# Kernel optimization log

Measured on AMD Instinct MI355X. Metric: run time of the kernel, lower is better.

## Reference

```python
import jax, jax.numpy as jnp
import numpy as np

B, D, OUT = 16384, 128, 32

def setup_inputs() -> dict:
    key = jax.random.key(0)
    kx, kw, kb = jax.random.split(key, 3)
    x = jax.random.normal(kx, (B, D), dtype=jnp.float32)
    # nn.Linear(in=D*(D+1), out=OUT): weight [OUT, D*(D+1)], bias [OUT]
    fan_in = D * (D + 1)
    bound = 1.0 / np.sqrt(fan_in)
    W = jax.random.uniform(kw, (OUT, fan_in), dtype=jnp.float32, minval=-bound, maxval=bound)
    b = jax.random.uniform(kb, (OUT,), dtype=jnp.float32, minval=-bound, maxval=bound)
    return {"x": x, "W": W, "b": b}

def reference(x, W, b):
    Bn, d = x.shape
    ones = jnp.ones((Bn, 1), dtype=x.dtype)
    xe = jnp.concatenate([x, ones], axis=-1)          # [B, d+1]
    # outer product z[b, i, j] = x[b, i] * xe[b, j]; flatten row-major -> [B, d*(d+1)]
    z = (x[:, :, None] * xe[:, None, :]).reshape(Bn, d * (d + 1))
    y = z @ W.T + b                                    # [B, OUT]
    return y
```

## Files before the change

kernel.cpp:

```cpp
#include <hip/hip_runtime.h>

typedef __attribute__((ext_vector_type(8)))  __bf16 bf16x8;
typedef __attribute__((ext_vector_type(16))) float  f32x16;
typedef unsigned int uint32;

#define D_IN  128
#define N_OUT 32
#define K129  129
#define WROW  16512
#define KE    144
#define NT    8
#define XQ_ELEMS (16384 * 128)
#define WQ_ELEMS (32 * 128 * KE)

__host__ __device__ __forceinline__ int permSlot(int s) {
    int q = s >> 3, h = (s >> 2) & 1, j = s & 3;
    return 16 * (q >> 1) + 8 * h + 4 * (q & 1) + j;
}

__global__ void prep(const float* __restrict__ x, const float* __restrict__ W,
                     __bf16* __restrict__ xq, __bf16* __restrict__ Wq) {
    int t = blockIdx.x * 256 + threadIdx.x;
    {
        const float4* s = reinterpret_cast<const float4*>(x) + (size_t)t * 2;
        float4 a = s[0], b = s[1];
        bf16x8 v = { (__bf16)a.x, (__bf16)a.y, (__bf16)a.z, (__bf16)a.w,
                     (__bf16)b.x, (__bf16)b.y, (__bf16)b.z, (__bf16)b.w };
        reinterpret_cast<bf16x8*>(xq)[t] = v;
    }
    for (int e = t; e < WQ_ELEMS; e += 262144) {
        int oi = e / KE, k = e - oi * KE;
        int o = oi >> 7, sg = oi & 127;
        int i = (sg & ~31) + permSlot(sg & 31);
        float v = (k <= D_IN) ? W[o * WROW + i * K129 + k] : 0.f;
        Wq[e] = (__bf16)v;
    }
}

#define STAGE(BUF, T)                                                              \
  do {                                                                             \
    if (PREP) {                                                                    \
      __builtin_amdgcn_global_load_lds(                                            \
        (const __attribute__((address_space(1))) uint32*)                          \
          (xq + ((rbase + (long)(T) * 32 + rs) * D_IN + cs * 8)),                  \
        (__attribute__((address_space(3))) uint32*)(&tile[BUF][wave * 512]),       \
        16, 0, 0);                                                                 \
    } else {                                                                       \
      const float* s0 = x + (rbase + (long)(T) * 32 + rs) * D_IN + cs * 8;         \
      float4 a0 = *(const float4*)s0, a1 = *(const float4*)(s0 + 4);               \
      bf16x8 v0 = { (__bf16)a0.x,(__bf16)a0.y,(__bf16)a0.z,(__bf16)a0.w,           \
                    (__bf16)a1.x,(__bf16)a1.y,(__bf16)a1.z,(__bf16)a1.w };         \
      *(bf16x8*)&tile[BUF][(size_t)tid * 8] = v0;                                  \
    }                                                                              \
  } while (0)

#define COMPUTE(BUF, MT)                                                           \
  {                                                                                \
    const char* tb = (const char*)&tile[BUF][0];                                   \
    bf16x8 Bf[8];                                                                  \
    _Pragma("unroll")                                                              \
    for (int ks = 0; ks < 8; ++ks)                                                 \
      Bf[ks] = *reinterpret_cast<const bf16x8*>(tb + laneB[ks]);                   \
    float sq[4] = {0.f, 0.f, 0.f, 0.f};                                            \
    __builtin_amdgcn_s_setprio(1);                                                 \
    _Pragma("unroll")                                                              \
    for (int ctl = 0; ctl < 2; ++ctl) {                                            \
      f32x16 a;                                                                    \
      _Pragma("unroll")                                                            \
      for (int r = 0; r < 16; ++r) a[r] = 0.f;                                     \
      _Pragma("unroll")                                                            \
      for (int ks = 0; ks < 8; ++ks)                                               \
        a = __builtin_amdgcn_mfma_f32_32x32x16_bf16(A[ctl][ks], Bf[ks], a, 0,0,0); \
      a = __builtin_amdgcn_mfma_f32_32x32x16_bf16(A[ctl][8], B8c, a, 0, 0, 0);     \
      if (sub == 0) {                                                              \
        _Pragma("unroll")                                                          \
        for (int q = 0; q < 4; ++q)                                                \
          _Pragma("unroll")                                                        \
          for (int j = 0; j < 4; ++j)                                              \
            sq[q] += a[q * 4 + j] * (float)Bf[2 * ctl + (q >> 1)][4 * (q & 1) + j];\
      } else {                                                                     \
        _Pragma("unroll")                                                          \
        for (int q = 0; q < 4; ++q)                                                \
          _Pragma("unroll")                                                        \
          for (int j = 0; j < 4; ++j)                                              \
            sq[q] += a[q*4 + j] * (float)Bf[4 + 2*ctl + (q >> 1)][4*(q & 1) + j];  \
      }                                                                            \
    }                                                                              \
    __builtin_amdgcn_s_setprio(0);                                                 \
    float s = (sq[0] + sq[1]) + (sq[2] + sq[3]);                                   \
    s += __shfl_xor(s, 32);                                                        \
    sArr[MT] = s;                                                                  \
  }

#define WAITV(N) asm volatile("s_waitcnt vmcnt(" #N ")" ::: "memory")

#define ITER(T, VN)                                                                \
  {                                                                                \
    WAITV(VN);                                                                     \
    __builtin_amdgcn_s_barrier();                                                  \
    asm volatile("" ::: "memory");                                                 \
    if ((T) + 3 < NT) STAGE(((T) + 3) & 3, (T) + 3);                               \
    COMPUTE((T) & 3, (T));                                                         \
  }

template<int PREP>
__global__ __launch_bounds__(512, 2) void quad10(
    const float* __restrict__ x, const float* __restrict__ W,
    const __bf16* __restrict__ xq, const __bf16* __restrict__ Wq,
    const float* __restrict__ bias, float* __restrict__ out)
{
    __shared__ __align__(16) __bf16 tile[4][32 * 128];
    __shared__ float red[4][2][NT][32];

    const int tid  = threadIdx.x;
    const int lane = tid & 63;
    const int wave = tid >> 6;
    const int o4   = wave >> 1;
    const int sub  = wave & 1;
    const int b32  = lane & 31, hi = lane >> 5;

    const int bid = blockIdx.x;
    const int xcd = bid & 7, idx = bid >> 3;
    const int run = xcd * 8 + (idx & 7);
    const int og  = idx >> 3;
    const int o   = og * 4 + o4;
    const long rbase = (long)run * (NT * 32);
    const float bias_o = bias[o];

    bf16x8 A[2][9];
    #pragma unroll
    for (int ctl = 0; ctl < 2; ++ctl) {
        const int g = sub * 2 + ctl;
        if (PREP) {
            const __bf16* base = Wq + ((size_t)o * 128 + g * 32 + b32) * KE + hi * 8;
            #pragma unroll
            for (int ks = 0; ks < 9; ++ks)
                A[ctl][ks] = *reinterpret_cast<const bf16x8*>(base + ks * 16);
        } else {
            const int i = g * 32 + permSlot(b32);
            const float* wr = W + (size_t)o * WROW + (size_t)i * K129;
            #pragma unroll
            for (int ks = 0; ks < 8; ++ks) {
                bf16x8 f;
                #pragma unroll
                for (int r = 0; r < 8; ++r) f[r] = (__bf16)wr[ks * 16 + hi * 8 + r];
                A[ctl][ks] = f;
            }
            bf16x8 f;
            #pragma unroll
            for (int r = 0; r < 8; ++r) f[r] = (__bf16)0.f;
            if (hi == 0) f[0] = (__bf16)wr[128];
            A[ctl][8] = f;
        }
    }

    bf16x8 B8c;
    #pragma unroll
    for (int r = 0; r < 8; ++r) B8c[r] = (__bf16)0.f;
    if (hi == 0) B8c[0] = (__bf16)1.0f;

    const int rs = tid >> 4, cs = (tid & 15) ^ (rs & 15);

    const int rm = b32 & 15;
    int laneB[8];
    #pragma unroll
    for (int ks = 0; ks < 8; ++ks)
        laneB[ks] = b32 * 256 + (((ks * 2 + hi) ^ rm) << 4);

    float sArr[NT];

    STAGE(0, 0);
    STAGE(1, 1);
    STAGE(2, 2);

    ITER(0, 2); ITER(1, 2); ITER(2, 2); ITER(3, 2);
    ITER(4, 2); ITER(5, 2); ITER(6, 1); ITER(7, 0);

    if (hi == 0) {
        #pragma unroll
        for (int mt = 0; mt < NT; ++mt) red[o4][sub][mt][b32] = sArr[mt];
    }
    __syncthreads();
    if (sub == 0 && hi == 0) {
        #pragma unroll
        for (int mt = 0; mt < NT; ++mt)
            out[(rbase + (long)mt * 32 + b32) * N_OUT + o] =
                red[o4][0][mt][b32] + red[o4][1][mt][b32] + bias_o;
    }
}

extern "C" void kernel_launch(void* const* d_in, const int* in_sizes, int n_in,
                              void* d_out, int out_size, void* d_ws, size_t ws_size,
                              hipStream_t stream) {
    const float* x    = (const float*)d_in[0];
    const float* W    = (const float*)d_in[1];
    const float* bias = (const float*)d_in[2];
    float* out = (float*)d_out;

    const size_t need = (size_t)(XQ_ELEMS + WQ_ELEMS) * sizeof(__bf16);
    if (ws_size >= need) {
        __bf16* xq = (__bf16*)d_ws;
        __bf16* Wq = xq + XQ_ELEMS;
        prep<<<1024, 256, 0, stream>>>(x, W, xq, Wq);
        quad10<1><<<512, 512, 0, stream>>>(x, W, xq, Wq, bias, out);
    } else {
        quad10<0><<<512, 512, 0, stream>>>(x, W, (const __bf16*)nullptr,
                                           (const __bf16*)nullptr, bias, out);
    }
}
```

Measured before the change: 32.53 us.

## Split main kernel into 256-thread blocks with triple buffering and vectorized W prep

The main kernel now uses 256-thread blocks that each cover two output columns instead of four, launched as 1024 blocks with a 3-deep LDS ring instead of 4, and each thread stages two x chunks. Per-tile partial sums go straight to shared memory instead of a register array. The prep kernel assigns W conversion to dedicated threads that write 8-wide bf16 vectors instead of a scalar strided loop. The aim is more resident blocks per CU and a cheaper prep pass, at the cost of shallower prefetch and duplicated x staging across more blocks.

```diff
diff --git a/kernel.cpp b/kernel.cpp
--- a/kernel.cpp
+++ b/kernel.cpp
@@ -21,19 +21,32 @@
 __global__ void prep(const float* __restrict__ x, const float* __restrict__ W,
                      __bf16* __restrict__ xq, __bf16* __restrict__ Wq) {
     int t = blockIdx.x * 256 + threadIdx.x;
-    {
+    if (t < 262144) {
         const float4* s = reinterpret_cast<const float4*>(x) + (size_t)t * 2;
         float4 a = s[0], b = s[1];
         bf16x8 v = { (__bf16)a.x, (__bf16)a.y, (__bf16)a.z, (__bf16)a.w,
                      (__bf16)b.x, (__bf16)b.y, (__bf16)b.z, (__bf16)b.w };
         reinterpret_cast<bf16x8*>(xq)[t] = v;
-    }
-    for (int e = t; e < WQ_ELEMS; e += 262144) {
-        int oi = e / KE, k = e - oi * KE;
+    } else if (t < 327680) {
+        int t2 = t - 262144;
+        int oi = t2 >> 4, oct = t2 & 15;
         int o = oi >> 7, sg = oi & 127;
         int i = (sg & ~31) + permSlot(sg & 31);
-        float v = (k <= D_IN) ? W[o * WROW + i * K129 + k] : 0.f;
-        Wq[e] = (__bf16)v;
+        const float* src = W + (size_t)o * WROW + (size_t)i * K129 + oct * 8;
+        bf16x8 v;
+        #pragma unroll
+        for (int r = 0; r < 8; ++r) v[r] = (__bf16)src[r];
+        *reinterpret_cast<bf16x8*>(Wq + (size_t)oi * KE + oct * 8) = v;
+    } else if (t < 335872) {
+        int t3 = t - 327680;
+        int oi = t3 >> 1, h = t3 & 1;
+        int o = oi >> 7, sg = oi & 127;
+        int i = (sg & ~31) + permSlot(sg & 31);
+        bf16x8 v;
+        #pragma unroll
+        for (int r = 0; r < 8; ++r) v[r] = (__bf16)0.f;
+        if (h == 0) v[0] = (__bf16)W[(size_t)o * WROW + (size_t)i * K129 + 128];
+        *reinterpret_cast<bf16x8*>(Wq + (size_t)oi * KE + 128 + h * 8) = v;
     }
 }
 
@@ -42,15 +55,22 @@
     if (PREP) {                                                                    \
       __builtin_amdgcn_global_load_lds(                                            \
         (const __attribute__((address_space(1))) uint32*)                          \
-          (xq + ((rbase + (long)(T) * 32 + rs) * D_IN + cs * 8)),                  \
-        (__attribute__((address_space(3))) uint32*)(&tile[BUF][wave * 512]),       \
+          (xq + ((rbase + (long)(T) * 32 + r0s) * D_IN + c0s * 8)),                \
+        (__attribute__((address_space(3))) uint32*)(&tile[BUF][wave * 1024]),      \
+        16, 0, 0);                                                                 \
+      __builtin_amdgcn_global_load_lds(                                            \
+        (const __attribute__((address_space(1))) uint32*)                          \
+          (xq + ((rbase + (long)(T) * 32 + r1s) * D_IN + c1s * 8)),                \
+        (__attribute__((address_space(3))) uint32*)(&tile[BUF][wave * 1024 + 512]),\
         16, 0, 0);                                                                 \
     } else {                                                                       \
-      const float* s0 = x + (rbase + (long)(T) * 32 + rs) * D_IN + cs * 8;         \
-      float4 a0 = *(const float4*)s0, a1 = *(const float4*)(s0 + 4);               \
-      bf16x8 v0 = { (__bf16)a0.x,(__bf16)a0.y,(__bf16)a0.z,(__bf16)a0.w,           \
-                    (__bf16)a1.x,(__bf16)a1.y,(__bf16)a1.z,(__bf16)a1.w };         \
-      *(bf16x8*)&tile[BUF][(size_t)tid * 8] = v0;                                  \
+      const float* s0 = x + (rbase + (long)(T) * 32 + r0s) * D_IN + c0s * 8;       \
+      const float* s1 = x + (rbase + (long)(T) * 32 + r1s) * D_IN + c1s * 8;       \
+      bf16x8 v0, v1;                                                               \
+      _Pragma("unroll")                                                            \
+      for (int r = 0; r < 8; ++r) { v0[r] = (__bf16)s0[r]; v1[r] = (__bf16)s1[r]; }\
+      *(bf16x8*)&tile[BUF][(size_t)p0 * 8] = v0;                                   \
+      *(bf16x8*)&tile[BUF][(size_t)p1 * 8] = v1;                                   \
     }                                                                              \
   } while (0)
 
@@ -89,41 +109,42 @@
     __builtin_amdgcn_s_setprio(0);                                                 \
     float s = (sq[0] + sq[1]) + (sq[2] + sq[3]);                                   \
     s += __shfl_xor(s, 32);                                                        \
-    sArr[MT] = s;                                                                  \
+    if (hi == 0) red[o2][sub][MT][b32] = s;                                        \
   }
 
 #define WAITV(N) asm volatile("s_waitcnt vmcnt(" #N ")" ::: "memory")
+#define DRAIN()  asm volatile("s_waitcnt vmcnt(0) lgkmcnt(0)" ::: "memory")
 
 #define ITER(T, VN)                                                                \
   {                                                                                \
-    WAITV(VN);                                                                     \
+    if (PREP) { WAITV(VN); } else { DRAIN(); }                                     \
     __builtin_amdgcn_s_barrier();                                                  \
     asm volatile("" ::: "memory");                                                 \
-    if ((T) + 3 < NT) STAGE(((T) + 3) & 3, (T) + 3);                               \
-    COMPUTE((T) & 3, (T));                                                         \
+    if ((T) + 2 < NT) STAGE(((T) + 2) % 3, (T) + 2);                               \
+    COMPUTE((T) % 3, (T));                                                         \
   }
 
 template<int PREP>
-__global__ __launch_bounds__(512, 2) void quad10(
+__global__ __launch_bounds__(256, 3) void quad11(
     const float* __restrict__ x, const float* __restrict__ W,
     const __bf16* __restrict__ xq, const __bf16* __restrict__ Wq,
     const float* __restrict__ bias, float* __restrict__ out)
 {
-    __shared__ __align__(16) __bf16 tile[4][32 * 128];
-    __shared__ float red[4][2][NT][32];
+    __shared__ __align__(16) __bf16 tile[3][32 * 128];
+    __shared__ float red[2][2][NT][32];
 
     const int tid  = threadIdx.x;
     const int lane = tid & 63;
     const int wave = tid >> 6;
-    const int o4   = wave >> 1;
+    const int o2   = wave >> 1;
     const int sub  = wave & 1;
     const int b32  = lane & 31, hi = lane >> 5;
 
     const int bid = blockIdx.x;
     const int xcd = bid & 7, idx = bid >> 3;
-    const int run = xcd * 8 + (idx & 7);
-    const int og  = idx >> 3;
-    const int o   = og * 4 + o4;
+    const int opair = idx & 15;
+    const int run = xcd * 8 + (idx >> 4);
+    const int o   = opair * 2 + o2;
     const long rbase = (long)run * (NT * 32);
     const float bias_o = bias[o];
 
@@ -159,7 +180,10 @@
     for (int r = 0; r < 8; ++r) B8c[r] = (__bf16)0.f;
     if (hi == 0) B8c[0] = (__bf16)1.0f;
 
-    const int rs = tid >> 4, cs = (tid & 15) ^ (rs & 15);
+    const int p0 = wave * 128 + lane;
+    const int r0s = p0 >> 4, c0s = (p0 & 15) ^ (r0s & 15);
+    const int p1 = p0 + 64;
+    const int r1s = p1 >> 4, c1s = (p1 & 15) ^ (r1s & 15);
 
     const int rm = b32 & 15;
     int laneB[8];
@@ -167,25 +191,20 @@
     for (int ks = 0; ks < 8; ++ks)
         laneB[ks] = b32 * 256 + (((ks * 2 + hi) ^ rm) << 4);
 
-    float sArr[NT];
-
     STAGE(0, 0);
     STAGE(1, 1);
-    STAGE(2, 2);
 
     ITER(0, 2); ITER(1, 2); ITER(2, 2); ITER(3, 2);
-    ITER(4, 2); ITER(5, 2); ITER(6, 1); ITER(7, 0);
-
-    if (hi == 0) {
+    ITER(4, 2); ITER(5, 2); ITER(6, 2); ITER(7, 0);
+
+    __syncthreads();
+    if (sub == 0) {
         #pragma unroll
-        for (int mt = 0; mt < NT; ++mt) red[o4][sub][mt][b32] = sArr[mt];
-    }
-    __syncthreads();
-    if (sub == 0 && hi == 0) {
-        #pragma unroll
-        for (int mt = 0; mt < NT; ++mt)
+        for (int m = 0; m < NT / 2; ++m) {
+            int mt = m * 2 + hi;
             out[(rbase + (long)mt * 32 + b32) * N_OUT + o] =
-                red[o4][0][mt][b32] + red[o4][1][mt][b32] + bias_o;
+                red[o2][0][mt][b32] + red[o2][1][mt][b32] + bias_o;
+        }
     }
 }
 
@@ -201,10 +220,10 @@
     if (ws_size >= need) {
         __bf16* xq = (__bf16*)d_ws;
         __bf16* Wq = xq + XQ_ELEMS;
-        prep<<<1024, 256, 0, stream>>>(x, W, xq, Wq);
-        quad10<1><<<512, 512, 0, stream>>>(x, W, xq, Wq, bias, out);
+        prep<<<1312, 256, 0, stream>>>(x, W, xq, Wq);
+        quad11<1><<<1024, 256, 0, stream>>>(x, W, xq, Wq, bias, out);
     } else {
-        quad10<0><<<512, 512, 0, stream>>>(x, W, (const __bf16*)nullptr,
-                                           (const __bf16*)nullptr, bias, out);
-    }
-}
+        quad11<0><<<1024, 256, 0, stream>>>(x, W, (const __bf16*)nullptr,
+                                            (const __bf16*)nullptr, bias, out);
+    }
+}
```

After: 31.28 us. 3.8% less time.
